# Kernel tuning notes

Measured on AMD Instinct MI355X. Metric: run time of the kernel, lower is better.

Reference implementation:

```python
import jax, jax.numpy as jnp
import numpy as np

HEADS = 16
KV_HEADS = 4
DIM_HEAD = 64
DIM = 1024
B, N = 2, 2048


def setup_inputs() -> dict:
    key = jax.random.key(0)
    k1, k2, k3 = jax.random.split(key, 3)
    x = jax.random.normal(k1, (B, N, DIM), dtype=jnp.float32)
    Wq = jax.random.normal(k2, (DIM, HEADS * DIM_HEAD), dtype=jnp.float32) / np.sqrt(DIM)
    Wkv = jax.random.normal(k3, (DIM, 2 * KV_HEADS * DIM_HEAD), dtype=jnp.float32) / np.sqrt(DIM)
    k_scale = jnp.ones((HEADS, 1, DIM_HEAD), dtype=jnp.float32)
    return {"x": x, "Wq": Wq, "Wkv": Wkv, "k_scale": k_scale}


def reference(x, Wq, Wkv, k_scale):
    b, n, _ = x.shape
    g = HEADS // KV_HEADS  # query heads per kv head
    scale = DIM_HEAD ** -0.5
    # fused qkv projections (no bias)
    q = (x @ Wq).reshape(b, n, HEADS, DIM_HEAD)
    kv = x @ Wkv
    k, v = jnp.split(kv, 2, axis=-1)
    k = k.reshape(b, n, KV_HEADS, DIM_HEAD).transpose(0, 2, 1, 3)  # b k n d
    v = v.reshape(b, n, KV_HEADS, DIM_HEAD).transpose(0, 2, 1, 3)  # b k n d
    # group query heads: b, kv_heads, g, n, d
    qg = q.transpose(0, 2, 1, 3).reshape(b, KV_HEADS, g, n, DIM_HEAD)
    # per-query-head k scale, applied to the group-broadcast k (qk-norm)
    ks = k_scale.reshape(KV_HEADS, g, 1, DIM_HEAD)
    kk = k[:, :, None, :, :] * ks  # b k g n d
    dots = jnp.einsum('bkgid,bkgjd->bkgij', qg, kk) * scale
    attn = jax.nn.softmax(dots, axis=-1)
    out = jnp.einsum('bkgij,bkjd->bkgid', attn, v)  # v broadcast over g
    out = out.reshape(b, HEADS, n, DIM_HEAD).transpose(0, 2, 1, 3).reshape(b, n, HEADS * DIM_HEAD)
    return out
```

## Files before the change

kernel.cpp:

```cpp
#include <hip/hip_runtime.h>
#include <stdint.h>
#include <math.h>

typedef __attribute__((ext_vector_type(8))) __bf16 bf16x8;
typedef __attribute__((ext_vector_type(4))) float f32x4;
typedef __attribute__((ext_vector_type(16))) float f32x16;

__device__ __forceinline__ uint32_t f32_to_bf16_rne(float f) {
  union { float f; uint32_t u; } v; v.f = f;
  return (v.u + 0x7FFFu + ((v.u >> 16) & 1u)) >> 16;
}

__device__ __forceinline__ uint32_t cvt_pk_bf16(float lo, float hi) {
  uint32_t r;
  asm("v_cvt_pk_bf16_f32 %0, %1, %2" : "=v"(r) : "v"(lo), "v"(hi));
  return r;
}

__device__ __forceinline__ void gld16(void* lds, const void* g) {
  __builtin_amdgcn_global_load_lds(
      (__attribute__((address_space(1))) void*)(g),
      (__attribute__((address_space(3))) void*)(lds), 16, 0, 0);
}

__device__ __forceinline__ f32x4 mfma16(bf16x8 a, bf16x8 b, f32x4 c) {
  return __builtin_amdgcn_mfma_f32_16x16x32_bf16(a, b, c, 0, 0, 0);
}
__device__ __forceinline__ f32x16 mfma32(bf16x8 a, bf16x8 b, f32x16 c) {
  return __builtin_amdgcn_mfma_f32_32x32x16_bf16(a, b, c, 0, 0, 0);
}

#define LOG2E 1.44269504088896340736f

__global__ __launch_bounds__(256) void k_convert_x(const float* __restrict__ x,
                                                   uint16_t* __restrict__ xb) {
  int i = blockIdx.x * 256 + threadIdx.x;
  const float4* xv = (const float4*)x;
  float4 a = xv[2 * i], b2 = xv[2 * i + 1];
  uint32_t w0 = f32_to_bf16_rne(a.x) | (f32_to_bf16_rne(a.y) << 16);
  uint32_t w1 = f32_to_bf16_rne(a.z) | (f32_to_bf16_rne(a.w) << 16);
  uint32_t w2 = f32_to_bf16_rne(b2.x) | (f32_to_bf16_rne(b2.y) << 16);
  uint32_t w3 = f32_to_bf16_rne(b2.z) | (f32_to_bf16_rne(b2.w) << 16);
  ((uint4*)xb)[i] = make_uint4(w0, w1, w2, w3);
}

__global__ __launch_bounds__(256) void k_convert_w(const float* __restrict__ wq,
                                                   const float* __restrict__ wkv,
                                                   uint16_t* __restrict__ wt) {
  __shared__ float tile[64][65];
  int c0 = blockIdx.x * 64, k0 = blockIdx.y * 64;
  int t = threadIdx.x;
  int col = t & 63, rq = t >> 6;
#pragma unroll
  for (int rr = 0; rr < 16; rr++) {
    int r = rr * 4 + rq;
    int c = c0 + col;
    float v = (c < 1024) ? wq[(uint64_t)(k0 + r) * 1024 + c]
                         : wkv[(uint64_t)(k0 + r) * 512 + (c - 1024)];
    tile[r][col] = v;
  }
  __syncthreads();
#pragma unroll
  for (int rr = 0; rr < 16; rr++) {
    int a = rr * 4 + rq;
    wt[(uint64_t)(c0 + a) * 1024 + k0 + col] = (uint16_t)f32_to_bf16_rne(tile[col][a]);
  }
}

__global__ __launch_bounds__(256, 3) void k_proj_gemm(
    const uint16_t* __restrict__ xb, const uint16_t* __restrict__ wt,
    const float* __restrict__ kscale, uint16_t* __restrict__ q_ws,
    uint16_t* __restrict__ kf_ws, uint16_t* __restrict__ vf_ws) {
  __shared__ __align__(16) uint16_t As[2][128 * 32];
  __shared__ __align__(16) uint16_t Bs[2][64 * 32];
  int t = threadIdx.x;
  int w = t >> 6, l = t & 63;
  int lq = l & 15, lg = l >> 4;
  int m0 = blockIdx.x * 128, n0 = blockIdx.y * 64;
  int wr = w >> 1, wc = w & 1;
  f32x4 acc[4][2] = {};

  auto stage = [&](int buf, int k0) {
#pragma unroll
    for (int j = 0; j < 2; j++) {
      int tt = j * 256 + t;
      int r = tt >> 2, s = tt & 3;
      int sl = s ^ ((r >> 1) & 3);
      gld16((char*)&As[buf][0] + (j * 256 + w * 64) * 16,
            xb + (uint64_t)(m0 + r) * 1024 + k0 + sl * 8);
    }
    {
      int r = t >> 2, s = t & 3;
      int sl = s ^ ((r >> 1) & 3);
      gld16((char*)&Bs[buf][0] + (w * 64) * 16,
            wt + (uint64_t)(n0 + r) * 1024 + k0 + sl * 8);
    }
  };

  stage(0, 0);
  asm volatile("s_waitcnt vmcnt(0)" ::: "memory");
  __builtin_amdgcn_s_barrier();
  int cur = 0;
  for (int k0 = 0; k0 < 1024; k0 += 32) {
    if (k0 + 32 < 1024) stage(cur ^ 1, k0 + 32);
    bf16x8 af[4], bfr[2];
#pragma unroll
    for (int m = 0; m < 4; m++) {
      int r = wr * 64 + m * 16 + lq;
      int s = lg ^ ((r >> 1) & 3);
      af[m] = *(const bf16x8*)(&As[cur][r * 32 + s * 8]);
    }
#pragma unroll
    for (int n = 0; n < 2; n++) {
      int r = wc * 32 + n * 16 + lq;
      int s = lg ^ ((r >> 1) & 3);
      bfr[n] = *(const bf16x8*)(&Bs[cur][r * 32 + s * 8]);
    }
    __builtin_amdgcn_s_setprio(1);
#pragma unroll
    for (int m = 0; m < 4; m++)
#pragma unroll
      for (int n = 0; n < 2; n++)
        acc[m][n] = mfma16(af[m], bfr[n], acc[m][n]);
    __builtin_amdgcn_s_setprio(0);
    asm volatile("s_waitcnt vmcnt(0) lgkmcnt(0)" ::: "memory");
    __builtin_amdgcn_s_barrier();
    cur ^= 1;
  }

#pragma unroll
  for (int m = 0; m < 4; m++)
#pragma unroll
    for (int n = 0; n < 2; n++)
#pragma unroll
      for (int jj = 0; jj < 4; jj++) {
        int row = m0 + wr * 64 + m * 16 + 4 * lg + jj;
        int col = n0 + wc * 32 + n * 16 + lq;
        float val = acc[m][n][jj];
        int b = row >> 11, nn = row & 2047;
        if (col < 1024) {
          val *= kscale[col] * 0.125f * LOG2E;
          q_ws[((uint64_t)((b * 16 + (col >> 6)) * 2048 + nn)) * 64 + (col & 63)] =
              (uint16_t)f32_to_bf16_rne(val);
        } else if (col < 1280) {
          int kvh = (col - 1024) >> 6;
          int d = col & 63;
          int kt = nn >> 6, st = (nn >> 5) & 1, lrr = nn & 31;
          int mm = d >> 4, hh = (d >> 3) & 1, el = d & 7;
          kf_ws[(uint64_t)(b * 4 + kvh) * 131072 +
                (uint64_t)((((kt * 8 + st * 4 + mm) * 64) + hh * 32 + lrr) * 8 + el)] =
              (uint16_t)f32_to_bf16_rne(val);
        } else {
          int kvh = (col - 1280) >> 6;
          int d = col & 63;
          int kt = nn >> 6, nl = nn & 63;
          int ss = nl >> 4, hh = (nl >> 3) & 1, el = nl & 7;
          int dd = d >> 5, lrr = d & 31;
          vf_ws[(uint64_t)(b * 4 + kvh) * 131072 +
                (uint64_t)((((kt * 8 + dd * 4 + ss) * 64) + hh * 32 + lrr) * 8 + el)] =
              (uint16_t)f32_to_bf16_rne(val);
        }
      }
}

__global__ __launch_bounds__(512, 4) void k_attn(const uint16_t* __restrict__ q_ws,
                                                 const uint16_t* __restrict__ kf_ws,
                                                 const uint16_t* __restrict__ vf_ws,
                                                 float* __restrict__ out) {
  __shared__ __align__(16) char smem[65536];

  int t = threadIdx.x, w = t >> 6, l = t & 63;
  int lr = l & 31, hi = l >> 5;
  int wq = w & 3, half = w >> 2;
  int blk = blockIdx.x;
  int c = blk & 7, j = blk >> 3;
  int b = c >> 2, kvh = c & 3;
  int h = kvh * 4 + (j >> 4), qb = j & 15;

  const uint16_t* Qb = q_ws + (uint64_t)(b * 16 + h) * 2048 * 64;
  const uint16_t* Kb = kf_ws + (uint64_t)(b * 4 + kvh) * 131072;
  const uint16_t* Vb = vf_ws + (uint64_t)(b * 4 + kvh) * 131072;
  int qrow0 = qb * 128 + wq * 32;

  bf16x8 qfrag[4];
#pragma unroll
  for (int m = 0; m < 4; m++)
    qfrag[m] = *(const bf16x8*)(Qb + (uint64_t)(qrow0 + lr) * 64 + m * 16 + hi * 8);

  f32x16 oacc[2] = {};
  float l_run = 0.f;

  char* KsBase = smem + half * 32768;
  char* VsBase = smem + half * 32768 + 16384;

  auto stageKV = [&](int buf, int kt) {
#pragma unroll
    for (int ii = 0; ii < 2; ii++) {
      int idx = wq * 2 + ii;
      gld16(KsBase + buf * 8192 + idx * 1024, Kb + (uint64_t)(kt * 8 + idx) * 512 + l * 8);
      gld16(VsBase + buf * 8192 + idx * 1024, Vb + (uint64_t)(kt * 8 + idx) * 512 + l * 8);
    }
  };

  int kt0 = half * 16;
  stageKV(0, kt0);
  asm volatile("s_waitcnt vmcnt(0)" ::: "memory");
  __builtin_amdgcn_s_barrier();
  int cur = 0;

  for (int it = 0; it < 16; it++) {
    if (it + 1 < 16) stageKV(cur ^ 1, kt0 + it + 1);
    const uint16_t* Ksc = (const uint16_t*)(KsBase + cur * 8192);
    const uint16_t* Vsc = (const uint16_t*)(VsBase + cur * 8192);

    f32x16 Tacc[2] = {};
    __builtin_amdgcn_s_setprio(1);
#pragma unroll
    for (int st = 0; st < 2; st++)
#pragma unroll
      for (int m = 0; m < 4; m++) {
        bf16x8 kf = *(const bf16x8*)(Ksc + (st * 4 + m) * 512 + l * 8);
        Tacc[st] = mfma32(kf, qfrag[m], Tacc[st]);
      }
    __builtin_amdgcn_s_setprio(0);

    float p[32];
#pragma unroll
    for (int e = 0; e < 16; e++) {
      p[e] = __builtin_amdgcn_exp2f(Tacc[0][e]);
      p[16 + e] = __builtin_amdgcn_exp2f(Tacc[1][e]);
    }
    float sm[8];
#pragma unroll
    for (int i = 0; i < 8; i++)
      sm[i] = (p[4 * i] + p[4 * i + 1]) + (p[4 * i + 2] + p[4 * i + 3]);
    float ls = ((sm[0] + sm[1]) + (sm[2] + sm[3])) + ((sm[4] + sm[5]) + (sm[6] + sm[7]));
    ls += __shfl_xor(ls, 32);
    l_run += ls;

    bf16x8 pa[4];
#pragma unroll
    for (int s = 0; s < 4; s++) {
      int base = (s >> 1) * 16 + (s & 1) * 8;
      uint32_t wlo0 = cvt_pk_bf16(p[base + 0], p[base + 1]);
      uint32_t wlo1 = cvt_pk_bf16(p[base + 2], p[base + 3]);
      uint32_t whi0 = cvt_pk_bf16(p[base + 4], p[base + 5]);
      uint32_t whi1 = cvt_pk_bf16(p[base + 6], p[base + 7]);
      uint32_t send0 = hi ? wlo0 : whi0;
      uint32_t send1 = hi ? wlo1 : whi1;
      uint32_t recv0 = (uint32_t)__shfl_xor((int)send0, 32);
      uint32_t recv1 = (uint32_t)__shfl_xor((int)send1, 32);
      union { uint32_t u[4]; bf16x8 v; } pu;
      pu.u[0] = hi ? recv0 : wlo0;
      pu.u[1] = hi ? recv1 : wlo1;
      pu.u[2] = hi ? whi0 : recv0;
      pu.u[3] = hi ? whi1 : recv1;
      pa[s] = pu.v;
    }

    __builtin_amdgcn_s_setprio(1);
#pragma unroll
    for (int dd = 0; dd < 2; dd++)
#pragma unroll
      for (int s = 0; s < 4; s++) {
        bf16x8 vf = *(const bf16x8*)(Vsc + (dd * 4 + s) * 512 + l * 8);
        oacc[dd] = mfma32(pa[s], vf, oacc[dd]);
      }
    __builtin_amdgcn_s_setprio(0);

    asm volatile("s_waitcnt vmcnt(0) lgkmcnt(0)" ::: "memory");
    __builtin_amdgcn_s_barrier();
    cur ^= 1;
  }

  float* exch = (float*)smem;
  float* exl = (float*)(smem + 32768);
  if (half == 1) {
#pragma unroll
    for (int r = 0; r < 16; r++) {
      int qr = (r & 3) + 8 * (r >> 2) + 4 * hi;
      exch[wq * 2048 + qr * 64 + lr] = oacc[0][r];
      exch[wq * 2048 + qr * 64 + 32 + lr] = oacc[1][r];
    }
    if (hi == 0) exl[wq * 32 + lr] = l_run;
  }
  __syncthreads();
  if (half == 0) {
    l_run += exl[wq * 32 + lr];
    float inv = 1.0f / l_run;
#pragma unroll
    for (int r = 0; r < 16; r++) {
      int qr = (r & 3) + 8 * (r >> 2) + 4 * hi;
      float iv = __shfl(inv, qr);
      float o0 = oacc[0][r] + exch[wq * 2048 + qr * 64 + lr];
      float o1 = oacc[1][r] + exch[wq * 2048 + qr * 64 + 32 + lr];
      float* orow = out + (uint64_t)(b * 2048 + qrow0 + qr) * 1024 + h * 64 + lr;
      orow[0] = o0 * iv;
      orow[32] = o1 * iv;
    }
  }
}

extern "C" void kernel_launch(void* const* d_in, const int* in_sizes, int n_in,
                              void* d_out, int out_size, void* d_ws, size_t ws_size,
                              hipStream_t stream) {
  const float* x = (const float*)d_in[0];
  const float* wq = (const float*)d_in[1];
  const float* wkv = (const float*)d_in[2];
  const float* kscale = (const float*)d_in[3];
  float* out = (float*)d_out;
  char* ws = (char*)d_ws;
  uint16_t* xb = (uint16_t*)(ws);
  uint16_t* wt = (uint16_t*)(ws + (8ull << 20));
  uint16_t* q_ws = (uint16_t*)(ws + (11ull << 20));
  uint16_t* kf_ws = (uint16_t*)(ws + (19ull << 20));
  uint16_t* vf_ws = (uint16_t*)(ws + (21ull << 20));

  k_convert_x<<<2048, 256, 0, stream>>>(x, xb);
  k_convert_w<<<dim3(24, 16), 256, 0, stream>>>(wq, wkv, wt);
  k_proj_gemm<<<dim3(32, 24), 256, 0, stream>>>(xb, wt, kscale, q_ws, kf_ws, vf_ws);
  k_attn<<<512, 512, 0, stream>>>(q_ws, kf_ws, vf_ws, out);
}
```

Baseline: 81.64 us.

## Load K/V fragments directly to registers, dropping LDS staging and barriers

Changes the K/V workspace layout to 32-key subtiles and has each wave load its K and V MFMA fragments straight from global memory into registers, with a one-step register prefetch. This removes the LDS double buffer and the per-iteration block barrier, and shrinks shared memory to what the final output exchange needs. The row-sum shuffle moves out of the loop. Each wave of the 4 query waves in a half now fetches the same K/V data separately, so global/L2 traffic rises, and load latency is hidden only by the single prefetch.

```diff
diff --git a/kernel.cpp b/kernel.cpp
--- a/kernel.cpp
+++ b/kernel.cpp
@@ -145,19 +145,18 @@
         } else if (col < 1280) {
           int kvh = (col - 1024) >> 6;
           int d = col & 63;
-          int kt = nn >> 6, st = (nn >> 5) & 1, lrr = nn & 31;
+          int gsu = nn >> 5, lrr = nn & 31;
           int mm = d >> 4, hh = (d >> 3) & 1, el = d & 7;
           kf_ws[(uint64_t)(b * 4 + kvh) * 131072 +
-                (uint64_t)((((kt * 8 + st * 4 + mm) * 64) + hh * 32 + lrr) * 8 + el)] =
+                (uint64_t)((((gsu * 4 + mm) * 64) + hh * 32 + lrr) * 8 + el)] =
               (uint16_t)f32_to_bf16_rne(val);
         } else {
           int kvh = (col - 1280) >> 6;
           int d = col & 63;
-          int kt = nn >> 6, nl = nn & 63;
-          int ss = nl >> 4, hh = (nl >> 3) & 1, el = nl & 7;
+          int gsu = nn >> 5, jj2 = (nn >> 4) & 1, hh = (nn >> 3) & 1, el = nn & 7;
           int dd = d >> 5, lrr = d & 31;
           vf_ws[(uint64_t)(b * 4 + kvh) * 131072 +
-                (uint64_t)((((kt * 8 + dd * 4 + ss) * 64) + hh * 32 + lrr) * 8 + el)] =
+                (uint64_t)((((gsu * 4 + dd * 2 + jj2) * 64) + hh * 32 + lrr) * 8 + el)] =
               (uint16_t)f32_to_bf16_rne(val);
         }
       }
@@ -167,7 +166,7 @@
                                                  const uint16_t* __restrict__ kf_ws,
                                                  const uint16_t* __restrict__ vf_ws,
                                                  float* __restrict__ out) {
-  __shared__ __align__(16) char smem[65536];
+  __shared__ __align__(16) char smem[33280];
 
   int t = threadIdx.x, w = t >> 6, l = t & 63;
   int lr = l & 31, hi = l >> 5;
@@ -178,8 +177,10 @@
   int h = kvh * 4 + (j >> 4), qb = j & 15;
 
   const uint16_t* Qb = q_ws + (uint64_t)(b * 16 + h) * 2048 * 64;
-  const uint16_t* Kb = kf_ws + (uint64_t)(b * 4 + kvh) * 131072;
-  const uint16_t* Vb = vf_ws + (uint64_t)(b * 4 + kvh) * 131072;
+  const uint16_t* Kp =
+      kf_ws + (uint64_t)(b * 4 + kvh) * 131072 + (uint64_t)half * 65536 + l * 8;
+  const uint16_t* Vp =
+      vf_ws + (uint64_t)(b * 4 + kvh) * 131072 + (uint64_t)half * 65536 + l * 8;
   int qrow0 = qb * 128 + wq * 32;
 
   bf16x8 qfrag[4];
@@ -190,58 +191,36 @@
   f32x16 oacc[2] = {};
   float l_run = 0.f;
 
-  char* KsBase = smem + half * 32768;
-  char* VsBase = smem + half * 32768 + 16384;
-
-  auto stageKV = [&](int buf, int kt) {
-#pragma unroll
-    for (int ii = 0; ii < 2; ii++) {
-      int idx = wq * 2 + ii;
-      gld16(KsBase + buf * 8192 + idx * 1024, Kb + (uint64_t)(kt * 8 + idx) * 512 + l * 8);
-      gld16(VsBase + buf * 8192 + idx * 1024, Vb + (uint64_t)(kt * 8 + idx) * 512 + l * 8);
-    }
-  };
-
-  int kt0 = half * 16;
-  stageKV(0, kt0);
-  asm volatile("s_waitcnt vmcnt(0)" ::: "memory");
-  __builtin_amdgcn_s_barrier();
-  int cur = 0;
-
-  for (int it = 0; it < 16; it++) {
-    if (it + 1 < 16) stageKV(cur ^ 1, kt0 + it + 1);
-    const uint16_t* Ksc = (const uint16_t*)(KsBase + cur * 8192);
-    const uint16_t* Vsc = (const uint16_t*)(VsBase + cur * 8192);
-
-    f32x16 Tacc[2] = {};
+  bf16x8 kf[4], vf[4];
+#pragma unroll
+  for (int i = 0; i < 4; i++) kf[i] = *(const bf16x8*)(Kp + i * 512);
+#pragma unroll
+  for (int i = 0; i < 4; i++) vf[i] = *(const bf16x8*)(Vp + i * 512);
+
+  for (int su = 0; su < 32; ++su) {
+    f32x16 Tacc = {};
     __builtin_amdgcn_s_setprio(1);
 #pragma unroll
-    for (int st = 0; st < 2; st++)
-#pragma unroll
-      for (int m = 0; m < 4; m++) {
-        bf16x8 kf = *(const bf16x8*)(Ksc + (st * 4 + m) * 512 + l * 8);
-        Tacc[st] = mfma32(kf, qfrag[m], Tacc[st]);
-      }
+    for (int m = 0; m < 4; m++) Tacc = mfma32(kf[m], qfrag[m], Tacc);
     __builtin_amdgcn_s_setprio(0);
 
-    float p[32];
-#pragma unroll
-    for (int e = 0; e < 16; e++) {
-      p[e] = __builtin_amdgcn_exp2f(Tacc[0][e]);
-      p[16 + e] = __builtin_amdgcn_exp2f(Tacc[1][e]);
-    }
-    float sm[8];
-#pragma unroll
-    for (int i = 0; i < 8; i++)
-      sm[i] = (p[4 * i] + p[4 * i + 1]) + (p[4 * i + 2] + p[4 * i + 3]);
-    float ls = ((sm[0] + sm[1]) + (sm[2] + sm[3])) + ((sm[4] + sm[5]) + (sm[6] + sm[7]));
-    ls += __shfl_xor(ls, 32);
-    l_run += ls;
-
-    bf16x8 pa[4];
-#pragma unroll
-    for (int s = 0; s < 4; s++) {
-      int base = (s >> 1) * 16 + (s & 1) * 8;
+    if (su != 31) {
+#pragma unroll
+      for (int i = 0; i < 4; i++)
+        kf[i] = *(const bf16x8*)(Kp + (su + 1) * 2048 + i * 512);
+    }
+
+    float p[16];
+#pragma unroll
+    for (int e = 0; e < 16; e++) p[e] = __builtin_amdgcn_exp2f(Tacc[e]);
+    float sm0 = ((p[0] + p[1]) + (p[2] + p[3])) + ((p[4] + p[5]) + (p[6] + p[7]));
+    float sm1 = ((p[8] + p[9]) + (p[10] + p[11])) + ((p[12] + p[13]) + (p[14] + p[15]));
+    l_run += sm0 + sm1;
+
+    bf16x8 pa[2];
+#pragma unroll
+    for (int jj = 0; jj < 2; jj++) {
+      int base = 8 * jj;
       uint32_t wlo0 = cvt_pk_bf16(p[base + 0], p[base + 1]);
       uint32_t wlo1 = cvt_pk_bf16(p[base + 2], p[base + 3]);
       uint32_t whi0 = cvt_pk_bf16(p[base + 4], p[base + 5]);
@@ -255,23 +234,25 @@
       pu.u[1] = hi ? recv1 : wlo1;
       pu.u[2] = hi ? whi0 : recv0;
       pu.u[3] = hi ? whi1 : recv1;
-      pa[s] = pu.v;
+      pa[jj] = pu.v;
     }
 
     __builtin_amdgcn_s_setprio(1);
 #pragma unroll
     for (int dd = 0; dd < 2; dd++)
 #pragma unroll
-      for (int s = 0; s < 4; s++) {
-        bf16x8 vf = *(const bf16x8*)(Vsc + (dd * 4 + s) * 512 + l * 8);
-        oacc[dd] = mfma32(pa[s], vf, oacc[dd]);
-      }
+      for (int jj = 0; jj < 2; jj++)
+        oacc[dd] = mfma32(pa[jj], vf[dd * 2 + jj], oacc[dd]);
     __builtin_amdgcn_s_setprio(0);
 
-    asm volatile("s_waitcnt vmcnt(0) lgkmcnt(0)" ::: "memory");
-    __builtin_amdgcn_s_barrier();
-    cur ^= 1;
-  }
+    if (su != 31) {
+#pragma unroll
+      for (int i = 0; i < 4; i++)
+        vf[i] = *(const bf16x8*)(Vp + (su + 1) * 2048 + i * 512);
+    }
+  }
+
+  l_run += __shfl_xor(l_run, 32);
 
   float* exch = (float*)smem;
   float* exl = (float*)(smem + 32768);
```

New measurement: 83.76 us. +2.6%, slower.
